# Performance work log

Hardware: AMD Instinct MI355X
Metric: run time of the kernel (lower is better)

Reference implementation:

```python
import jax, jax.numpy as jnp
import numpy as np

N = 100000
E = 3200000
F_IN = 256
HID = 128


def _dconv_k1(x_cat, w, b):
    # torch_geometric_temporal DConv with K=1:
    # H = X @ W[0,0] + X @ W[1,0] + b   (no graph propagation for K=1)
    return x_cat @ (w[0, 0] + w[1, 0]) + b


def _dcrnn_cell(x, h, wz, bz, wr, br, wh, bh):
    xh = jnp.concatenate([x, h], axis=1)
    z = jax.nn.sigmoid(_dconv_k1(xh, wz, bz))
    r = jax.nn.sigmoid(_dconv_k1(xh, wr, br))
    xrh = jnp.concatenate([x, r * h], axis=1)
    h_tilde = jnp.tanh(_dconv_k1(xrh, wh, bh))
    return z * h + (1.0 - z) * h_tilde


def setup_inputs() -> dict:
    key = jax.random.key(0)
    ks = jax.random.split(key, 16)

    def gw(k, shape):
        fan_in = shape[-2]
        return jax.random.normal(k, shape, dtype=jnp.float32) / np.sqrt(fan_in)

    inp = {
        "x": jax.random.normal(ks[0], (N, F_IN), dtype=jnp.float32),
        "edge_index": jax.random.randint(ks[1], (2, E), 0, N, dtype=jnp.int64 if jax.config.jax_enable_x64 else jnp.int32),
        "edge_weight": jax.random.uniform(ks[2], (E,), dtype=jnp.float32),
        "w_z1": gw(ks[3], (2, 1, F_IN + HID, HID)), "b_z1": jnp.zeros((HID,), jnp.float32),
        "w_r1": gw(ks[4], (2, 1, F_IN + HID, HID)), "b_r1": jnp.zeros((HID,), jnp.float32),
        "w_h1": gw(ks[5], (2, 1, F_IN + HID, HID)), "b_h1": jnp.zeros((HID,), jnp.float32),
        "w_z2": gw(ks[6], (2, 1, HID + HID // 2, HID // 2)), "b_z2": jnp.zeros((HID // 2,), jnp.float32),
        "w_r2": gw(ks[7], (2, 1, HID + HID // 2, HID // 2)), "b_r2": jnp.zeros((HID // 2,), jnp.float32),
        "w_h2": gw(ks[8], (2, 1, HID + HID // 2, HID // 2)), "b_h2": jnp.zeros((HID // 2,), jnp.float32),
        "w_lin1": gw(ks[9], (HID // 2, 16)), "b_lin1": jnp.zeros((16,), jnp.float32),
        "w_lin2": gw(ks[10], (16, 1)), "b_lin2": jnp.zeros((1,), jnp.float32),
    }
    return inp


def reference(x, edge_index, edge_weight,
              w_z1, b_z1, w_r1, b_r1, w_h1, b_h1,
              w_z2, b_z2, w_r2, b_r2, w_h2, b_h2,
              w_lin1, b_lin1, w_lin2, b_lin2):
    # edge_index / edge_weight are unused in the K=1 DConv math (faithful to tgt source).
    h0 = jnp.zeros((x.shape[0], w_z1.shape[-1]), x.dtype)
    h = _dcrnn_cell(x, h0, w_z1, b_z1, w_r1, b_r1, w_h1, b_h1)
    h = jax.nn.relu(h)
    h0b = jnp.zeros((x.shape[0], w_z2.shape[-1]), x.dtype)
    h = _dcrnn_cell(h, h0b, w_z2, b_z2, w_r2, b_r2, w_h2, b_h2)
    h = jax.nn.relu(h)
    # Dropout(0.2) is identity at inference
    h = jax.nn.relu(h @ w_lin1 + b_lin1)
    return h @ w_lin2 + b_lin2
```

## Files before the change

kernel.cpp:

```cpp
#include <hip/hip_runtime.h>

typedef _Float16 f16;
typedef _Float16 f16x4 __attribute__((ext_vector_type(4)));
typedef _Float16 f16x8 __attribute__((ext_vector_type(8)));
typedef float    f32x4 __attribute__((ext_vector_type(4)));

#define N_ROWS 100000
#define RT 782

#define W1T_OFF 0
#define W1T_BYTES (256 * 256 * 2)
#define W2T_OFF W1T_BYTES

#define A_XS 0
#define A_WS 18432
#define A_H1 0
#define A_W2 36864
#define A_H2 0
#define ARENA_BYTES 69632
#define LSX 72
#define LSH1 136
#define LSH2 72

__device__ __forceinline__ void glds16(const void* g, void* l) {
    __builtin_amdgcn_global_load_lds((const __attribute__((address_space(1))) void*)g,
                                     (__attribute__((address_space(3))) void*)l, 16, 0, 0);
}

__global__ void prep_w1(const float* __restrict__ wz, const float* __restrict__ wh,
                        f16* __restrict__ W1T) {
    int idx = blockIdx.x * 256 + threadIdx.x;
    int k = idx >> 8;
    int c = idx & 255;
    const float* w = (c < 128) ? wz : wh;
    int cc = c & 127;
    float v = w[k * 128 + cc] + w[384 * 128 + k * 128 + cc];
    W1T[c * 256 + k] = (f16)v;
}

__global__ void prep_w2(const float* __restrict__ wz, const float* __restrict__ wh,
                        f16* __restrict__ W2T) {
    int idx = blockIdx.x * 256 + threadIdx.x;
    int k = idx >> 7;
    int c = idx & 127;
    const float* w = (c < 64) ? wz : wh;
    int cc = c & 63;
    float v = w[k * 64 + cc] + w[192 * 64 + k * 64 + cc];
    W2T[c * 128 + k] = (f16)v;
}

__global__ __launch_bounds__(256, 2) void fused(
    const float* __restrict__ x,
    const f16* __restrict__ W1T, const f16* __restrict__ W2T,
    const float* __restrict__ bz1, const float* __restrict__ bh1,
    const float* __restrict__ bz2, const float* __restrict__ bh2,
    const float* __restrict__ wl1, const float* __restrict__ bl1,
    const float* __restrict__ wl2, const float* __restrict__ bl2,
    float* __restrict__ out)
{
    __shared__ __align__(16) char arena[ARENA_BYTES];
    const int tid = threadIdx.x, lane = tid & 63, wave = tid >> 6;
    const int ln = lane & 15, quad = lane >> 4;
    const int rh = wave >> 1, jh = wave & 1;
    const int r0 = blockIdx.x * 128;

    f16* Xs = (f16*)(arena + A_XS);
    f16* Ws = (f16*)(arena + A_WS);

    float4 xa[4], xb[4];

#define X_LOAD(KB)                                                               \
    _Pragma("unroll")                                                            \
    for (int it2 = 0; it2 < 4; ++it2) {                                          \
        const int idx = (it2 << 8) + tid;                                        \
        const int row = idx >> 3, cc = idx & 7;                                  \
        const int gr = (r0 + row < N_ROWS) ? (r0 + row) : (N_ROWS - 1);          \
        const float* xp = x + (size_t)gr * 256 + (KB) + (cc << 3);               \
        xa[it2] = *(const float4*)xp;                                            \
        xb[it2] = *(const float4*)(xp + 4);                                      \
    }

    X_LOAD(0)

    f32x4 acc[8][4];
#pragma unroll
    for (int a = 0; a < 8; ++a)
#pragma unroll
        for (int b = 0; b < 4; ++b) acc[a][b] = (f32x4){0.f, 0.f, 0.f, 0.f};

    const int wrloc = lane >> 3, wslot = lane & 7;

    for (int kb = 0; kb < 256; kb += 64) {
#pragma unroll
        for (int it2 = 0; it2 < 4; ++it2) {
            const int idx = (it2 << 8) + tid;
            const int row = idx >> 3, cc = idx & 7;
            f16x8 p = {(f16)xa[it2].x, (f16)xa[it2].y, (f16)xa[it2].z, (f16)xa[it2].w,
                       (f16)xb[it2].x, (f16)xb[it2].y, (f16)xb[it2].z, (f16)xb[it2].w};
            *(f16x8*)&Xs[row * LSX + (cc << 3)] = p;
        }
#pragma unroll
        for (int c = 0; c < 8; ++c) {
            const int h = wave * 8 + c;
            const int col = h * 8 + wrloc;
            glds16(W1T + (size_t)col * 256 + kb + ((wslot ^ (col & 7)) << 3),
                   Ws + h * 512);
        }
        __syncthreads();
        if (kb < 192) { X_LOAD(kb + 64) }

#pragma unroll
        for (int kc = 0; kc < 2; ++kc) {
            f16x8 bf[4];
#pragma unroll
            for (int nt = 0; nt < 4; ++nt)
                bf[nt] = *(const f16x8*)&Xs[((rh << 6) + (nt << 4) + ln) * LSX + kc * 32 + quad * 8];
            const int sw = ((kc * 4 + quad) ^ (ln & 7)) << 3;
#pragma unroll
            for (int mt = 0; mt < 8; ++mt) {
                const int col = ((mt & 3) << 4) + (jh << 6) + ((mt >> 2) << 7) + ln;
                f16x8 af = *(const f16x8*)&Ws[col * 64 + sw];
#pragma unroll
                for (int nt = 0; nt < 4; ++nt)
                    acc[mt][nt] = __builtin_amdgcn_mfma_f32_16x16x32_f16(af, bf[nt], acc[mt][nt], 0, 0, 0);
            }
        }
        __syncthreads();
    }
#undef X_LOAD

    f16* h1s = (f16*)(arena + A_H1);
#pragma unroll
    for (int mtp = 0; mtp < 4; ++mtp) {
        const int jg0 = (jh << 6) + (mtp << 4) + (quad << 2);
        const float4 zb4 = *(const float4*)(bz1 + jg0);
        const float4 hb4 = *(const float4*)(bh1 + jg0);
        const float zbv[4] = {zb4.x, zb4.y, zb4.z, zb4.w};
        const float hbv[4] = {hb4.x, hb4.y, hb4.z, hb4.w};
#pragma unroll
        for (int nt = 0; nt < 4; ++nt) {
            const int row = (rh << 6) + (nt << 4) + ln;
            f16x4 pk;
#pragma unroll
            for (int i = 0; i < 4; ++i) {
                float zp = acc[mtp][nt][i] + zbv[i];
                float hp = acc[mtp + 4][nt][i] + hbv[i];
                float ex = __expf(2.0f * hp);
                float th = 1.0f - 2.0f / (ex + 1.0f);
                float sg = 1.0f / (1.0f + __expf(zp));
                pk[i] = (f16)fmaxf(th * sg, 0.0f);
            }
            *(f16x4*)&h1s[row * LSH1 + jg0] = pk;
        }
    }

    f16* W2s = (f16*)(arena + A_W2);
    {
        const int rloc = lane >> 4, s = lane & 15;
#pragma unroll
        for (int c = 0; c < 8; ++c) {
            const int h = wave * 8 + c;
            const int col = h * 4 + rloc;
            glds16(W2T + (size_t)col * 128 + ((s ^ (col & 15)) << 3), W2s + h * 512);
        }
    }
    __syncthreads();

    f32x4 acc2[4][4];
#pragma unroll
    for (int a = 0; a < 4; ++a)
#pragma unroll
        for (int b = 0; b < 4; ++b) acc2[a][b] = (f32x4){0.f, 0.f, 0.f, 0.f};

#pragma unroll
    for (int kc = 0; kc < 4; ++kc) {
        f16x8 bf[4];
#pragma unroll
        for (int nt = 0; nt < 4; ++nt)
            bf[nt] = *(const f16x8*)&h1s[((rh << 6) + (nt << 4) + ln) * LSH1 + kc * 32 + quad * 8];
        const int sw = ((kc * 4 + quad) ^ ln) << 3;
#pragma unroll
        for (int mt = 0; mt < 4; ++mt) {
            const int col = ((mt & 1) << 4) + (jh << 5) + ((mt >> 1) << 6) + ln;
            f16x8 af = *(const f16x8*)&W2s[col * 128 + sw];
#pragma unroll
            for (int nt = 0; nt < 4; ++nt)
                acc2[mt][nt] = __builtin_amdgcn_mfma_f32_16x16x32_f16(af, bf[nt], acc2[mt][nt], 0, 0, 0);
        }
    }
    __syncthreads();

    f16* h2s = (f16*)(arena + A_H2);
#pragma unroll
    for (int mtp = 0; mtp < 2; ++mtp) {
        const int jg0 = (jh << 5) + (mtp << 4) + (quad << 2);
        const float4 zb4 = *(const float4*)(bz2 + jg0);
        const float4 hb4 = *(const float4*)(bh2 + jg0);
        const float zbv[4] = {zb4.x, zb4.y, zb4.z, zb4.w};
        const float hbv[4] = {hb4.x, hb4.y, hb4.z, hb4.w};
#pragma unroll
        for (int nt = 0; nt < 4; ++nt) {
            const int row = (rh << 6) + (nt << 4) + ln;
            f16x4 pk;
#pragma unroll
            for (int i = 0; i < 4; ++i) {
                float zp = acc2[mtp][nt][i] + zbv[i];
                float hp = acc2[mtp + 2][nt][i] + hbv[i];
                float ex = __expf(2.0f * hp);
                float th = 1.0f - 2.0f / (ex + 1.0f);
                float sg = 1.0f / (1.0f + __expf(zp));
                pk[i] = (f16)fmaxf(th * sg, 0.0f);
            }
            *(f16x4*)&h2s[row * LSH2 + jg0] = pk;
        }
    }
    __syncthreads();

    const float blv  = bl1[ln];
    const float wlv  = wl2[ln];
    const float bl2v = bl2[0];
    f16x8 bfr[2];
#pragma unroll
    for (int kc = 0; kc < 2; ++kc)
#pragma unroll
        for (int j = 0; j < 8; ++j)
            bfr[kc][j] = (f16)wl1[(kc * 32 + quad * 8 + j) * 16 + ln];

    f32x4 acc3[2] = {(f32x4){0.f, 0.f, 0.f, 0.f}, (f32x4){0.f, 0.f, 0.f, 0.f}};
#pragma unroll
    for (int t2 = 0; t2 < 2; ++t2)
#pragma unroll
        for (int kc = 0; kc < 2; ++kc) {
            f16x8 af = *(const f16x8*)&h2s[((wave << 5) + (t2 << 4) + ln) * LSH2 + kc * 32 + quad * 8];
            acc3[t2] = __builtin_amdgcn_mfma_f32_16x16x32_f16(af, bfr[kc], acc3[t2], 0, 0, 0);
        }

#pragma unroll
    for (int t2 = 0; t2 < 2; ++t2)
#pragma unroll
        for (int i = 0; i < 4; ++i) {
            float v = fmaxf(acc3[t2][i] + blv, 0.0f) * wlv;
            v += __shfl_xor(v, 1);
            v += __shfl_xor(v, 2);
            v += __shfl_xor(v, 4);
            v += __shfl_xor(v, 8);
            if (ln == 0) {
                const int row = r0 + (wave << 5) + (t2 << 4) + (quad << 2) + i;
                if (row < N_ROWS) out[row] = v + bl2v;
            }
        }
}

extern "C" void kernel_launch(void* const* d_in, const int* in_sizes, int n_in,
                              void* d_out, int out_size, void* d_ws, size_t ws_size,
                              hipStream_t stream) {
    const float* x   = (const float*)d_in[0];
    const float* wz1 = (const float*)d_in[3];
    const float* bz1 = (const float*)d_in[4];
    const float* wh1 = (const float*)d_in[7];
    const float* bh1 = (const float*)d_in[8];
    const float* wz2 = (const float*)d_in[9];
    const float* bz2 = (const float*)d_in[10];
    const float* wh2 = (const float*)d_in[13];
    const float* bh2 = (const float*)d_in[14];
    const float* wl1 = (const float*)d_in[15];
    const float* bl1 = (const float*)d_in[16];
    const float* wl2 = (const float*)d_in[17];
    const float* bl2 = (const float*)d_in[18];

    char* ws = (char*)d_ws;
    f16* W1T = (f16*)(ws + W1T_OFF);
    f16* W2T = (f16*)(ws + W2T_OFF);
    float* out = (float*)d_out;

    prep_w1<<<256, 256, 0, stream>>>(wz1, wh1, W1T);
    prep_w2<<<64, 256, 0, stream>>>(wz2, wh2, W2T);
    fused<<<RT, 256, 0, stream>>>(x, W1T, W2T, bz1, bh1, bz2, bh2,
                                  wl1, bl1, wl2, bl2, out);
}
```

Measured before the change: 246.7 us.

## Load GEMM operands directly from global into registers, halve row tile

Drops LDS staging of x and weight tiles. Each wave now loads its x rows and W1T/W2T fragments straight from global into registers, with a one-step software prefetch across the k loop. The row tile shrinks from 128 to 64 per block, which doubles the grid, and the two weight-prep kernels are merged into one launch. This removes LDS traffic and per-k barriers but reloads the weights from L2 for every block and gives up LDS-based reuse of x and W across waves.

```diff
diff --git a/kernel.cpp b/kernel.cpp
--- a/kernel.cpp
+++ b/kernel.cpp
@@ -6,47 +6,31 @@
 typedef float    f32x4 __attribute__((ext_vector_type(4)));
 
 #define N_ROWS 100000
-#define RT 782
+#define RT 1563
+#define LSH1 136
+#define LSH2 72
 
 #define W1T_OFF 0
 #define W1T_BYTES (256 * 256 * 2)
 #define W2T_OFF W1T_BYTES
 
-#define A_XS 0
-#define A_WS 18432
-#define A_H1 0
-#define A_W2 36864
-#define A_H2 0
-#define ARENA_BYTES 69632
-#define LSX 72
-#define LSH1 136
-#define LSH2 72
-
-__device__ __forceinline__ void glds16(const void* g, void* l) {
-    __builtin_amdgcn_global_load_lds((const __attribute__((address_space(1))) void*)g,
-                                     (__attribute__((address_space(3))) void*)l, 16, 0, 0);
-}
-
-__global__ void prep_w1(const float* __restrict__ wz, const float* __restrict__ wh,
-                        f16* __restrict__ W1T) {
-    int idx = blockIdx.x * 256 + threadIdx.x;
-    int k = idx >> 8;
-    int c = idx & 255;
-    const float* w = (c < 128) ? wz : wh;
-    int cc = c & 127;
-    float v = w[k * 128 + cc] + w[384 * 128 + k * 128 + cc];
-    W1T[c * 256 + k] = (f16)v;
-}
-
-__global__ void prep_w2(const float* __restrict__ wz, const float* __restrict__ wh,
-                        f16* __restrict__ W2T) {
-    int idx = blockIdx.x * 256 + threadIdx.x;
-    int k = idx >> 7;
-    int c = idx & 127;
-    const float* w = (c < 64) ? wz : wh;
-    int cc = c & 63;
-    float v = w[k * 64 + cc] + w[192 * 64 + k * 64 + cc];
-    W2T[c * 128 + k] = (f16)v;
+__global__ void prep_w(const float* __restrict__ wz1, const float* __restrict__ wh1,
+                       const float* __restrict__ wz2, const float* __restrict__ wh2,
+                       f16* __restrict__ W1T, f16* __restrict__ W2T) {
+    const int b = blockIdx.x;
+    if (b < 256) {
+        int idx = b * 256 + threadIdx.x;
+        int k = idx >> 8, c = idx & 255;
+        const float* w = (c < 128) ? wz1 : wh1;
+        int cc = c & 127;
+        W1T[c * 256 + k] = (f16)(w[k * 128 + cc] + w[384 * 128 + k * 128 + cc]);
+    } else {
+        int idx = (b - 256) * 256 + threadIdx.x;
+        int k = idx >> 7, c = idx & 127;
+        const float* w = (c < 64) ? wz2 : wh2;
+        int cc = c & 63;
+        W2T[c * 128 + k] = (f16)(w[k * 64 + cc] + w[192 * 64 + k * 64 + cc]);
+    }
 }
 
 __global__ __launch_bounds__(256, 2) void fused(
@@ -58,88 +42,77 @@
     const float* __restrict__ wl2, const float* __restrict__ bl2,
     float* __restrict__ out)
 {
-    __shared__ __align__(16) char arena[ARENA_BYTES];
+    __shared__ __align__(16) f16 h1s[64 * LSH1];
+    __shared__ __align__(16) f16 h2s[64 * LSH2];
+
     const int tid = threadIdx.x, lane = tid & 63, wave = tid >> 6;
     const int ln = lane & 15, quad = lane >> 4;
     const int rh = wave >> 1, jh = wave & 1;
-    const int r0 = blockIdx.x * 128;
-
-    f16* Xs = (f16*)(arena + A_XS);
-    f16* Ws = (f16*)(arena + A_WS);
-
-    float4 xa[4], xb[4];
-
-#define X_LOAD(KB)                                                               \
-    _Pragma("unroll")                                                            \
-    for (int it2 = 0; it2 < 4; ++it2) {                                          \
-        const int idx = (it2 << 8) + tid;                                        \
-        const int row = idx >> 3, cc = idx & 7;                                  \
-        const int gr = (r0 + row < N_ROWS) ? (r0 + row) : (N_ROWS - 1);          \
-        const float* xp = x + (size_t)gr * 256 + (KB) + (cc << 3);               \
-        xa[it2] = *(const float4*)xp;                                            \
-        xb[it2] = *(const float4*)(xp + 4);                                      \
-    }
-
-    X_LOAD(0)
-
-    f32x4 acc[8][4];
+    const int r0 = blockIdx.x * 64;
+    const int jgq = quad << 2;
+
+    const float* xbase[2];
+#pragma unroll
+    for (int nt = 0; nt < 2; ++nt) {
+        int gr = r0 + 32 * rh + 16 * nt + ln;
+        if (gr >= N_ROWS) gr = N_ROWS - 1;
+        xbase[nt] = x + (size_t)gr * 256 + quad * 8;
+    }
+    const f16* wbase[8];
+#pragma unroll
+    for (int mt = 0; mt < 8; ++mt) {
+        const int col = ((mt & 3) << 4) + (jh << 6) + ((mt >> 2) << 7) + ln;
+        wbase[mt] = W1T + col * 256 + quad * 8;
+    }
+
+    f32x4 acc[8][2];
 #pragma unroll
     for (int a = 0; a < 8; ++a)
 #pragma unroll
-        for (int b = 0; b < 4; ++b) acc[a][b] = (f32x4){0.f, 0.f, 0.f, 0.f};
-
-    const int wrloc = lane >> 3, wslot = lane & 7;
-
-    for (int kb = 0; kb < 256; kb += 64) {
-#pragma unroll
-        for (int it2 = 0; it2 < 4; ++it2) {
-            const int idx = (it2 << 8) + tid;
-            const int row = idx >> 3, cc = idx & 7;
-            f16x8 p = {(f16)xa[it2].x, (f16)xa[it2].y, (f16)xa[it2].z, (f16)xa[it2].w,
-                       (f16)xb[it2].x, (f16)xb[it2].y, (f16)xb[it2].z, (f16)xb[it2].w};
-            *(f16x8*)&Xs[row * LSX + (cc << 3)] = p;
-        }
-#pragma unroll
-        for (int c = 0; c < 8; ++c) {
-            const int h = wave * 8 + c;
-            const int col = h * 8 + wrloc;
-            glds16(W1T + (size_t)col * 256 + kb + ((wslot ^ (col & 7)) << 3),
-                   Ws + h * 512);
-        }
-        __syncthreads();
-        if (kb < 192) { X_LOAD(kb + 64) }
-
-#pragma unroll
-        for (int kc = 0; kc < 2; ++kc) {
-            f16x8 bf[4];
-#pragma unroll
-            for (int nt = 0; nt < 4; ++nt)
-                bf[nt] = *(const f16x8*)&Xs[((rh << 6) + (nt << 4) + ln) * LSX + kc * 32 + quad * 8];
-            const int sw = ((kc * 4 + quad) ^ (ln & 7)) << 3;
-#pragma unroll
-            for (int mt = 0; mt < 8; ++mt) {
-                const int col = ((mt & 3) << 4) + (jh << 6) + ((mt >> 2) << 7) + ln;
-                f16x8 af = *(const f16x8*)&Ws[col * 64 + sw];
-#pragma unroll
-                for (int nt = 0; nt < 4; ++nt)
-                    acc[mt][nt] = __builtin_amdgcn_mfma_f32_16x16x32_f16(af, bf[nt], acc[mt][nt], 0, 0, 0);
-            }
-        }
-        __syncthreads();
-    }
-#undef X_LOAD
-
-    f16* h1s = (f16*)(arena + A_H1);
+        for (int b = 0; b < 2; ++b) acc[a][b] = (f32x4){0.f, 0.f, 0.f, 0.f};
+
+#define P1_LOAD(DXA, DXB, DW, KC)                                \
+    _Pragma("unroll") for (int nt = 0; nt < 2; ++nt) {           \
+        DXA[nt] = *(const float4*)(xbase[nt] + (KC) * 32);       \
+        DXB[nt] = *(const float4*)(xbase[nt] + (KC) * 32 + 4);   \
+    }                                                            \
+    _Pragma("unroll") for (int mt = 0; mt < 8; ++mt)             \
+        DW[mt] = *(const f16x8*)(wbase[mt] + (KC) * 32);
+
+    float4 cxa[2], cxb[2]; f16x8 cw[8];
+    P1_LOAD(cxa, cxb, cw, 0)
+
+#pragma unroll
+    for (int kc = 0; kc < 8; ++kc) {
+        float4 nxa[2], nxb[2]; f16x8 nw[8];
+        if (kc < 7) { P1_LOAD(nxa, nxb, nw, kc + 1) }
+        f16x8 bf[2];
+#pragma unroll
+        for (int nt = 0; nt < 2; ++nt)
+            bf[nt] = (f16x8){(f16)cxa[nt].x, (f16)cxa[nt].y, (f16)cxa[nt].z, (f16)cxa[nt].w,
+                             (f16)cxb[nt].x, (f16)cxb[nt].y, (f16)cxb[nt].z, (f16)cxb[nt].w};
+#pragma unroll
+        for (int mt = 0; mt < 8; ++mt)
+#pragma unroll
+            for (int nt = 0; nt < 2; ++nt)
+                acc[mt][nt] = __builtin_amdgcn_mfma_f32_16x16x32_f16(cw[mt], bf[nt], acc[mt][nt], 0, 0, 0);
+#pragma unroll
+        for (int nt = 0; nt < 2; ++nt) { cxa[nt] = nxa[nt]; cxb[nt] = nxb[nt]; }
+#pragma unroll
+        for (int mt = 0; mt < 8; ++mt) cw[mt] = nw[mt];
+    }
+#undef P1_LOAD
+
 #pragma unroll
     for (int mtp = 0; mtp < 4; ++mtp) {
-        const int jg0 = (jh << 6) + (mtp << 4) + (quad << 2);
-        const float4 zb4 = *(const float4*)(bz1 + jg0);
-        const float4 hb4 = *(const float4*)(bh1 + jg0);
-        const float zbv[4] = {zb4.x, zb4.y, zb4.z, zb4.w};
-        const float hbv[4] = {hb4.x, hb4.y, hb4.z, hb4.w};
-#pragma unroll
-        for (int nt = 0; nt < 4; ++nt) {
-            const int row = (rh << 6) + (nt << 4) + ln;
+        const int jg0 = (jh << 6) + (mtp << 4) + jgq;
+        const float4 zb = *(const float4*)(bz1 + jg0);
+        const float4 hb = *(const float4*)(bh1 + jg0);
+        const float zbv[4] = {zb.x, zb.y, zb.z, zb.w};
+        const float hbv[4] = {hb.x, hb.y, hb.z, hb.w};
+#pragma unroll
+        for (int nt = 0; nt < 2; ++nt) {
+            const int row = 32 * rh + 16 * nt + ln;
             f16x4 pk;
 #pragma unroll
             for (int i = 0; i < 4; ++i) {
@@ -153,54 +126,45 @@
             *(f16x4*)&h1s[row * LSH1 + jg0] = pk;
         }
     }
-
-    f16* W2s = (f16*)(arena + A_W2);
-    {
-        const int rloc = lane >> 4, s = lane & 15;
-#pragma unroll
-        for (int c = 0; c < 8; ++c) {
-            const int h = wave * 8 + c;
-            const int col = h * 4 + rloc;
-            glds16(W2T + (size_t)col * 128 + ((s ^ (col & 15)) << 3), W2s + h * 512);
-        }
-    }
     __syncthreads();
 
-    f32x4 acc2[4][4];
+    const f16* w2base[4];
+#pragma unroll
+    for (int mt = 0; mt < 4; ++mt) {
+        const int col = ((mt & 1) << 4) + (jh << 5) + ((mt >> 1) << 6) + ln;
+        w2base[mt] = W2T + col * 128 + quad * 8;
+    }
+    f32x4 acc2[4][2];
 #pragma unroll
     for (int a = 0; a < 4; ++a)
 #pragma unroll
-        for (int b = 0; b < 4; ++b) acc2[a][b] = (f32x4){0.f, 0.f, 0.f, 0.f};
+        for (int b = 0; b < 2; ++b) acc2[a][b] = (f32x4){0.f, 0.f, 0.f, 0.f};
 
 #pragma unroll
     for (int kc = 0; kc < 4; ++kc) {
-        f16x8 bf[4];
-#pragma unroll
-        for (int nt = 0; nt < 4; ++nt)
-            bf[nt] = *(const f16x8*)&h1s[((rh << 6) + (nt << 4) + ln) * LSH1 + kc * 32 + quad * 8];
-        const int sw = ((kc * 4 + quad) ^ ln) << 3;
+        f16x8 bf[2];
+#pragma unroll
+        for (int nt = 0; nt < 2; ++nt)
+            bf[nt] = *(const f16x8*)&h1s[(32 * rh + 16 * nt + ln) * LSH1 + kc * 32 + quad * 8];
 #pragma unroll
         for (int mt = 0; mt < 4; ++mt) {
-            const int col = ((mt & 1) << 4) + (jh << 5) + ((mt >> 1) << 6) + ln;
-            f16x8 af = *(const f16x8*)&W2s[col * 128 + sw];
-#pragma unroll
-            for (int nt = 0; nt < 4; ++nt)
+            f16x8 af = *(const f16x8*)(w2base[mt] + kc * 32);
+#pragma unroll
+            for (int nt = 0; nt < 2; ++nt)
                 acc2[mt][nt] = __builtin_amdgcn_mfma_f32_16x16x32_f16(af, bf[nt], acc2[mt][nt], 0, 0, 0);
         }
     }
-    __syncthreads();
-
-    f16* h2s = (f16*)(arena + A_H2);
+
 #pragma unroll
     for (int mtp = 0; mtp < 2; ++mtp) {
-        const int jg0 = (jh << 5) + (mtp << 4) + (quad << 2);
-        const float4 zb4 = *(const float4*)(bz2 + jg0);
-        const float4 hb4 = *(const float4*)(bh2 + jg0);
-        const float zbv[4] = {zb4.x, zb4.y, zb4.z, zb4.w};
-        const float hbv[4] = {hb4.x, hb4.y, hb4.z, hb4.w};
-#pragma unroll
-        for (int nt = 0; nt < 4; ++nt) {
-            const int row = (rh << 6) + (nt << 4) + ln;
+        const int jg0 = (jh << 5) + (mtp << 4) + jgq;
+        const float4 zb = *(const float4*)(bz2 + jg0);
+        const float4 hb = *(const float4*)(bh2 + jg0);
+        const float zbv[4] = {zb.x, zb.y, zb.z, zb.w};
+        const float hbv[4] = {hb.x, hb.y, hb.z, hb.w};
+#pragma unroll
+        for (int nt = 0; nt < 2; ++nt) {
+            const int row = 32 * rh + 16 * nt + ln;
             f16x4 pk;
 #pragma unroll
             for (int i = 0; i < 4; ++i) {
@@ -226,29 +190,25 @@
         for (int j = 0; j < 8; ++j)
             bfr[kc][j] = (f16)wl1[(kc * 32 + quad * 8 + j) * 16 + ln];
 
-    f32x4 acc3[2] = {(f32x4){0.f, 0.f, 0.f, 0.f}, (f32x4){0.f, 0.f, 0.f, 0.f}};
-#pragma unroll
-    for (int t2 = 0; t2 < 2; ++t2)
-#pragma unroll
-        for (int kc = 0; kc < 2; ++kc) {
-            f16x8 af = *(const f16x8*)&h2s[((wave << 5) + (t2 << 4) + ln) * LSH2 + kc * 32 + quad * 8];
-            acc3[t2] = __builtin_amdgcn_mfma_f32_16x16x32_f16(af, bfr[kc], acc3[t2], 0, 0, 0);
-        }
-
-#pragma unroll
-    for (int t2 = 0; t2 < 2; ++t2)
-#pragma unroll
-        for (int i = 0; i < 4; ++i) {
-            float v = fmaxf(acc3[t2][i] + blv, 0.0f) * wlv;
-            v += __shfl_xor(v, 1);
-            v += __shfl_xor(v, 2);
-            v += __shfl_xor(v, 4);
-            v += __shfl_xor(v, 8);
-            if (ln == 0) {
-                const int row = r0 + (wave << 5) + (t2 << 4) + (quad << 2) + i;
-                if (row < N_ROWS) out[row] = v + bl2v;
-            }
-        }
+    f32x4 acc3 = (f32x4){0.f, 0.f, 0.f, 0.f};
+#pragma unroll
+    for (int kc = 0; kc < 2; ++kc) {
+        f16x8 af = *(const f16x8*)&h2s[(16 * wave + ln) * LSH2 + kc * 32 + quad * 8];
+        acc3 = __builtin_amdgcn_mfma_f32_16x16x32_f16(af, bfr[kc], acc3, 0, 0, 0);
+    }
+
+#pragma unroll
+    for (int i = 0; i < 4; ++i) {
+        float v = fmaxf(acc3[i] + blv, 0.0f) * wlv;
+        v += __shfl_xor(v, 1);
+        v += __shfl_xor(v, 2);
+        v += __shfl_xor(v, 4);
+        v += __shfl_xor(v, 8);
+        if (ln == 0) {
+            const int row = r0 + 16 * wave + (quad << 2) + i;
+            if (row < N_ROWS) out[row] = v + bl2v;
+        }
+    }
 }
 
 extern "C" void kernel_launch(void* const* d_in, const int* in_sizes, int n_in,
@@ -273,8 +233,7 @@
     f16* W2T = (f16*)(ws + W2T_OFF);
     float* out = (float*)d_out;
 
-    prep_w1<<<256, 256, 0, stream>>>(wz1, wh1, W1T);
-    prep_w2<<<64, 256, 0, stream>>>(wz2, wh2, W2T);
+    prep_w<<<320, 256, 0, stream>>>(wz1, wh1, wz2, wh2, W1T, W2T);
     fused<<<RT, 256, 0, stream>>>(x, W1T, W2T, bz1, bh1, bz2, bh2,
                                   wl1, bl1, wl2, bl2, out);
 }
```

Measured after the change: 277.6 us. 12.5% more time.
